# Performance work log

Measured on AMD Instinct MI355X. Metric: run time of the kernel, lower is better.

## Reference

```python
import jax, jax.numpy as jnp
import numpy as np

NUM_NODES = 100000
EMBED_DIM = 128
HIDDEN = 128
NUM_EDGES = 1600000


def gcn_conv(x, W, b, src, dst, num_nodes):
    """PyG GCNConv: x' = D^{-1/2} (A+I) D^{-1/2} (x W) + b, symmetric norm with self-loops."""
    x = x @ W  # [N, out]
    loops = jnp.arange(num_nodes, dtype=src.dtype)
    s = jnp.concatenate([src, loops])  # sources incl. self-loops
    d = jnp.concatenate([dst, loops])  # targets incl. self-loops
    deg = jax.ops.segment_sum(jnp.ones_like(d, dtype=x.dtype), d, num_segments=num_nodes)
    dis = jnp.where(deg > 0, jax.lax.rsqrt(deg), 0.0)  # deg^{-1/2}, 0 where isolated
    norm = dis[s] * dis[d]  # [E+N]
    msg = x[s] * norm[:, None]  # gather + scale
    out = jax.ops.segment_sum(msg, d, num_segments=num_nodes)  # scatter-add
    return out + b


def setup_inputs() -> dict:
    key = jax.random.key(0)
    k1, k2, k3, k4, k5, k6 = jax.random.split(key, 6)
    edge_index = jax.random.randint(k1, (2, NUM_EDGES), 0, NUM_NODES, dtype=jnp.int64)
    edge_attr = jax.random.normal(k2, (NUM_EDGES,), dtype=jnp.float32)
    emb = jax.random.normal(k3, (NUM_NODES, EMBED_DIM), dtype=jnp.float32) * 0.1
    W1 = jax.random.normal(k4, (EMBED_DIM, HIDDEN), dtype=jnp.float32) * (1.0 / np.sqrt(EMBED_DIM))
    b1 = jnp.zeros((HIDDEN,), dtype=jnp.float32)
    W2 = jax.random.normal(k5, (HIDDEN, HIDDEN), dtype=jnp.float32) * (1.0 / np.sqrt(HIDDEN))
    b2 = jnp.zeros((HIDDEN,), dtype=jnp.float32)
    return {"edge_index": edge_index, "edge_attr": edge_attr, "emb": emb,
            "W1": W1, "b1": b1, "W2": W2, "b2": b2}


def reference(edge_index, edge_attr, emb, W1, b1, W2, b2):
    src, dst = edge_index[0], edge_index[1]
    x = gcn_conv(emb, W1, b1, src, dst, NUM_NODES)
    x = jax.nn.relu(x)
    x = gcn_conv(x, W2, b2, src, dst, NUM_NODES)
    return x
```

## Files before the change

kernel.cpp:

```cpp
#include <hip/hip_runtime.h>

#define EMB 128
#define NBUC 1024
#define NPART 256
#define PREPB 128

typedef __attribute__((ext_vector_type(8))) short short8;
typedef __attribute__((ext_vector_type(4))) float f32x4;

__device__ __forceinline__ unsigned short f2bf(float f) {
    union { float f; unsigned int i; } v; v.f = f;
    unsigned int x = v.i;
    x += 0x7fffu + ((x >> 16) & 1u);
    return (unsigned short)(x >> 16);
}
__device__ __forceinline__ void acc_fma4(uint2 v, float d,
                                         float& a0, float& a1, float& a2, float& a3) {
    union { unsigned int i; float f; } t;
    t.i = v.x << 16;          a0 = fmaf(d, t.f, a0);
    t.i = v.x & 0xffff0000u;  a1 = fmaf(d, t.f, a1);
    t.i = v.y << 16;          a2 = fmaf(d, t.f, a2);
    t.i = v.y & 0xffff0000u;  a3 = fmaf(d, t.f, a3);
}
__device__ __forceinline__ void acc_bf4(uint2 v,
                                        float& a0, float& a1, float& a2, float& a3) {
    union { unsigned int i; float f; } t;
    t.i = v.x << 16;          a0 += t.f;
    t.i = v.x & 0xffff0000u;  a1 += t.f;
    t.i = v.y << 16;          a2 += t.f;
    t.i = v.y & 0xffff0000u;  a3 += t.f;
}


__device__ __forceinline__ void p1_body(int bid, int* h, const int* __restrict__ dst,
                                        int* __restrict__ tot, int E, int chunk) {
    for (int i = threadIdx.x; i < NBUC; i += 256) h[i] = 0;
    __syncthreads();
    int s = bid * chunk;
    int e = min(E, s + chunk);
    for (int i = s + threadIdx.x; i < e; i += 256)
        atomicAdd(&h[dst[i] >> 7], 1);
    __syncthreads();
    for (int i = threadIdx.x; i < NBUC; i += 256) {
        int v = h[i];
        if (v) atomicAdd(&tot[i], v);
    }
}

__device__ __forceinline__ void prepw_body(int bid, const float* __restrict__ W1,
                                           const float* __restrict__ W2,
                                           unsigned short* __restrict__ W1s,
                                           unsigned short* __restrict__ W2s) {
    int gid = bid * 256 + threadIdx.x;
    const float* W = (gid < 16384) ? W1 : W2;
    unsigned short* Ws = (gid < 16384) ? W1s : W2s;
    int idx = gid & 16383;
    int k = idx >> 7, n = idx & 127;
    int kk = k >> 5, q = (k >> 3) & 3, j = k & 7;
    int ct = n >> 4, nn = n & 15;
    int didx = ((((kk * 8 + ct) * 4 + q) * 16 + nn) << 3) + j;
    Ws[didx] = f2bf(W[idx]);
}

__global__ __launch_bounds__(256) void k_start(const int* __restrict__ dst,
                                               int* __restrict__ tot, int E, int chunk,
                                               const float* __restrict__ W1,
                                               const float* __restrict__ W2,
                                               unsigned short* __restrict__ W1s,
                                               unsigned short* __restrict__ W2s) {
    __shared__ int h[NBUC];
    int b = blockIdx.x;
    if (b < NPART) p1_body(b, h, dst, tot, E, chunk);
    else           prepw_body(b - NPART, W1, W2, W1s, W2s);
}

__global__ __launch_bounds__(1024) void p_scan(const int* __restrict__ tot,
                                               int* __restrict__ base,
                                               int* __restrict__ gcnt, int E) {
    __shared__ int a[NBUC];
    int t = threadIdx.x;
    int v0 = tot[t];
    a[t] = v0;
    __syncthreads();
    for (int off = 1; off < NBUC; off <<= 1) {
        int v = (t >= off) ? a[t - off] : 0;
        __syncthreads();
        a[t] += v;
        __syncthreads();
    }
    int excl = a[t] - v0;
    base[t] = excl;
    gcnt[t] = excl;
    if (t == NBUC - 1) base[NBUC] = E;
}

__device__ __forceinline__ void scatter_body(int bid, int* cnt,
                                             const int* __restrict__ src,
                                             const int* __restrict__ dst,
                                             int* __restrict__ gcnt,
                                             int* __restrict__ part,
                                             int E, int chunk) {
    for (int i = threadIdx.x; i < NBUC; i += 256) cnt[i] = 0;
    __syncthreads();
    int s = bid * chunk;
    int e = min(E, s + chunk);
    for (int i = s + threadIdx.x; i < e; i += 256)
        atomicAdd(&cnt[dst[i] >> 7], 1);
    __syncthreads();
    for (int i = threadIdx.x; i < NBUC; i += 256) {
        int c = cnt[i];
        cnt[i] = c ? atomicAdd(&gcnt[i], c) : 0;
    }
    __syncthreads();
    for (int i = s + threadIdx.x; i < e; i += 256) {
        int d = dst[i];
        int pos = atomicAdd(&cnt[d >> 7], 1);
        part[pos] = src[i] | ((d & 127) << 17);
    }
}

__global__ __launch_bounds__(256) void p3_csr(const int* __restrict__ part,
                                              const int* __restrict__ base,
                                              int* __restrict__ R, int* __restrict__ adj,
                                              float* __restrict__ dis, int N, int E) {
    __shared__ int hist[128];
    __shared__ int sc[128];
    __shared__ int cnt[128];
    int b = blockIdx.x;
    int n0 = b * 128;
    int nn = min(128, N - n0);
    int s = base[b], e = base[b + 1];
    int t = threadIdx.x;

    if (t < 128) hist[t] = 0;
    __syncthreads();
    for (int i = s + t; i < e; i += 256)
        atomicAdd(&hist[part[i] >> 17], 1);
    __syncthreads();

    if (t < 128) sc[t] = hist[t];
    __syncthreads();
    for (int off = 1; off < 128; off <<= 1) {
        int v = 0;
        if (t < 128 && t >= off) v = sc[t - off];
        __syncthreads();
        if (t < 128) sc[t] += v;
        __syncthreads();
    }
    if (t < 128) {
        int excl = sc[t] - hist[t];
        cnt[t] = excl;
        if (t < nn) {
            R[n0 + t] = s + excl;
            dis[n0 + t] = rsqrtf((float)hist[t] + 1.0f);
        }
    }
    if (b == 0 && t == 0) R[N] = E;
    __syncthreads();

    for (int i = s + t; i < e; i += 256) {
        int p = part[i];
        int pos = atomicAdd(&cnt[p >> 17], 1);
        adj[s + pos] = p & 0x1FFFF;
    }
}

template <bool XBF16, bool SCALE>
__device__ __forceinline__ void gemm_body(int bid, unsigned short* lds,
    const void* Xv, const unsigned short* __restrict__ Wsw,
    const float* __restrict__ dis, unsigned short* __restrict__ Y, int N)
{
    {
        const uint4* srcp = (const uint4*)Wsw;
        uint4* dstp = (uint4*)lds;
        for (int i = threadIdx.x; i < 2048; i += 256) dstp[i] = srcp[i];
    }
    __syncthreads();

    const int wave = threadIdx.x >> 6;
    const int lane = threadIdx.x & 63;
    const int q = lane >> 4, nn = lane & 15;
    const int row0 = bid * 64 + wave * 16;
    const int arow = row0 + nn;
    const int arc = arow < N ? arow : N - 1;

    f32x4 acc[8];
#pragma unroll
    for (int ct = 0; ct < 8; ++ct) acc[ct] = (f32x4){0.f, 0.f, 0.f, 0.f};

#pragma unroll
    for (int kk = 0; kk < 4; ++kk) {
        short8 af;
        if (XBF16) {
            af = *(const short8*)((const unsigned short*)Xv + (size_t)arc * EMB + kk * 32 + q * 8);
        } else {
            const float* xp = (const float*)Xv + (size_t)arc * EMB + kk * 32 + q * 8;
            float4 u0 = *(const float4*)xp;
            float4 u1 = *(const float4*)(xp + 4);
            af[0] = (short)f2bf(u0.x); af[1] = (short)f2bf(u0.y);
            af[2] = (short)f2bf(u0.z); af[3] = (short)f2bf(u0.w);
            af[4] = (short)f2bf(u1.x); af[5] = (short)f2bf(u1.y);
            af[6] = (short)f2bf(u1.z); af[7] = (short)f2bf(u1.w);
        }
#pragma unroll
        for (int ct = 0; ct < 8; ++ct) {
            short8 bf = ((const short8*)lds)[(kk * 8 + ct) * 64 + lane];
            acc[ct] = __builtin_amdgcn_mfma_f32_16x16x32_bf16(af, bf, acc[ct], 0, 0, 0);
        }
    }

    __syncthreads();

    float dv[4];
    if (SCALE) {
#pragma unroll
        for (int r = 0; r < 4; ++r) {
            int gm = row0 + q * 4 + r;
            dv[r] = dis[gm < N ? gm : N - 1];
        }
    }
#pragma unroll
    for (int ct = 0; ct < 8; ++ct) {
#pragma unroll
        for (int r = 0; r < 4; ++r) {
            int ml = wave * 16 + q * 4 + r;
            float val = SCALE ? acc[ct][r] * dv[r] : acc[ct][r];
            lds[ml * 136 + ct * 16 + nn] = f2bf(val);
        }
    }
    __syncthreads();

    const int rbase = bid * 64;
    for (int i = threadIdx.x; i < 1024; i += 256) {
        int row = i >> 4, off = i & 15;
        int grow = rbase + row;
        if (grow < N) {
            uint4 v = *(const uint4*)(lds + row * 136 + off * 8);
            *((uint4*)(Y + (size_t)grow * EMB) + off) = v;
        }
    }
}

__global__ __launch_bounds__(256) void k_mid(
    const int* __restrict__ src, const int* __restrict__ dstp,
    int* __restrict__ gcnt, int* __restrict__ part, int E, int chunk,
    const void* Xv, const unsigned short* __restrict__ W1s,
    unsigned short* __restrict__ Y, int N)
{
    __shared__ __align__(16) unsigned short smem[16384];
    int b = blockIdx.x;
    if (b < NPART) scatter_body(b, (int*)smem, src, dstp, gcnt, part, E, chunk);
    else           gemm_body<false, false>(b - NPART, smem, Xv, W1s, nullptr, Y, N);
}

__global__ __launch_bounds__(256) void k_gemm2(
    const void* Xv, const unsigned short* __restrict__ Wsw,
    const float* __restrict__ dis, unsigned short* __restrict__ Y, int N)
{
    __shared__ __align__(16) unsigned short smem[16384];
    gemm_body<true, true>(blockIdx.x, smem, Xv, Wsw, dis, Y, N);
}

template <bool FOLD, bool RELU, bool BF16OUT>
__global__ __launch_bounds__(256) void k_gather_split(
    const int* __restrict__ R, const int* __restrict__ adj,
    const unsigned short* __restrict__ Y, const float* __restrict__ dis,
    const float* __restrict__ bias, void* __restrict__ Outv, int N, int half)
{
    int bid = blockIdx.x;
    int pass = (bid >= half) ? 1 : 0;
    int t = (bid - pass * half) * 256 + threadIdx.x;
    int n = t >> 4;
    if (n >= N) return;
    int j = pass * 64 + (t & 15) * 4;

    int rs = R[n], re = R[n + 1];
    float dv = dis[n];

    float a0 = 0.f, a1 = 0.f, a2 = 0.f, a3 = 0.f;
    uint2 sv = *(const uint2*)(Y + (size_t)n * EMB + j);
    if (FOLD) acc_fma4(sv, dv, a0, a1, a2, a3);
    else      acc_bf4(sv, a0, a1, a2, a3);

    int e = rs;
    for (; e + 3 < re; e += 4) {
        int s0 = adj[e], s1 = adj[e + 1], s2 = adj[e + 2], s3 = adj[e + 3];
        uint2 v0 = *(const uint2*)(Y + (size_t)s0 * EMB + j);
        uint2 v1 = *(const uint2*)(Y + (size_t)s1 * EMB + j);
        uint2 v2 = *(const uint2*)(Y + (size_t)s2 * EMB + j);
        uint2 v3 = *(const uint2*)(Y + (size_t)s3 * EMB + j);
        if (FOLD) {
            float d0 = dis[s0], d1 = dis[s1], d2 = dis[s2], d3 = dis[s3];
            acc_fma4(v0, d0, a0, a1, a2, a3); acc_fma4(v1, d1, a0, a1, a2, a3);
            acc_fma4(v2, d2, a0, a1, a2, a3); acc_fma4(v3, d3, a0, a1, a2, a3);
        } else {
            acc_bf4(v0, a0, a1, a2, a3); acc_bf4(v1, a0, a1, a2, a3);
            acc_bf4(v2, a0, a1, a2, a3); acc_bf4(v3, a0, a1, a2, a3);
        }
    }
    for (; e < re; ++e) {
        int s0 = adj[e];
        uint2 v0 = *(const uint2*)(Y + (size_t)s0 * EMB + j);
        if (FOLD) acc_fma4(v0, dis[s0], a0, a1, a2, a3);
        else      acc_bf4(v0, a0, a1, a2, a3);
    }

    float4 b = *(const float4*)(bias + j);
    float o0 = dv * a0 + b.x;
    float o1 = dv * a1 + b.y;
    float o2 = dv * a2 + b.z;
    float o3 = dv * a3 + b.w;
    if (RELU) {
        o0 = fmaxf(o0, 0.f); o1 = fmaxf(o1, 0.f);
        o2 = fmaxf(o2, 0.f); o3 = fmaxf(o3, 0.f);
    }
    if (BF16OUT) {
        ushort4 o = { f2bf(o0), f2bf(o1), f2bf(o2), f2bf(o3) };
        *(ushort4*)((unsigned short*)Outv + (size_t)n * EMB + j) = o;
    } else {
        float4 o = { o0, o1, o2, o3 };
        *(float4*)((float*)Outv + (size_t)n * EMB + j) = o;
    }
}

extern "C" void kernel_launch(void* const* d_in, const int* in_sizes, int n_in,
                              void* d_out, int out_size, void* d_ws, size_t ws_size,
                              hipStream_t stream) {
    const int* ei = (const int*)d_in[0];
    const int E = in_sizes[0] / 2;
    const float* emb = (const float*)d_in[2];
    const int N = in_sizes[2] / EMB;
    const float* W1 = (const float*)d_in[3];
    const float* b1 = (const float*)d_in[4];
    const float* W2 = (const float*)d_in[5];
    const float* b2 = (const float*)d_in[6];
    float* out = (float*)d_out;

    const int* src = ei;
    const int* dstp = ei + E;

    char* w = (char*)d_ws;
    auto take = [&](size_t bytes) { char* p = w; w += (bytes + 511) & ~(size_t)511; return p; };
    float* dis  = (float*)take((size_t)N * 4);
    int*   R    = (int*)  take((size_t)(N + 1) * 4);
    int*   base = (int*)  take((size_t)(NBUC + 1) * 4);
    int*   tot  = (int*)  take((size_t)NBUC * 4);
    int*   gcnt = (int*)  take((size_t)NBUC * 4);
    int*   adj  = (int*)  take((size_t)E * 4);
    unsigned short* W1s = (unsigned short*)take((size_t)EMB * EMB * 2);
    unsigned short* W2s = (unsigned short*)take((size_t)EMB * EMB * 2);
    unsigned short* Hb  = (unsigned short*)take((size_t)N * EMB * 2);
    int*   part = (int*)Hb;
    unsigned short* Y1b = (unsigned short*)d_out;

    const int NB = (N + 127) / 128;
    const int chunk = (E + NPART - 1) / NPART;
    const int gM = (N + 63) / 64;
    const int half = (N * 16 + 255) / 256;
    const int gG = 2 * half;

    hipMemsetAsync(tot, 0, (size_t)NBUC * 4, stream);

    k_start<<<NPART + PREPB, 256, 0, stream>>>(dstp, tot, E, chunk, W1, W2, W1s, W2s);

    p_scan<<<1, NBUC, 0, stream>>>(tot, base, gcnt, E);

    k_mid<<<NPART + gM, 256, 0, stream>>>(src, dstp, gcnt, part, E, chunk,
                                          emb, W1s, Y1b, N);

    p3_csr<<<NB, 256, 0, stream>>>(part, base, R, adj, dis, N, E);

    k_gather_split<true, true, true><<<gG, 256, 0, stream>>>(R, adj, Y1b, dis, b1, Hb, N, half);

    k_gemm2<<<gM, 256, 0, stream>>>(Hb, W2s, dis, Hb, N);
    k_gather_split<false, false, false><<<gG, 256, 0, stream>>>(R, adj, Hb, dis, b2, out, N, half);
}
```

Before: 325.6 us.

## Fuse first-layer aggregation with second GEMM and widen gathers to full rows

The layer-1 gather, bias and ReLU now feed straight into the layer-2 MFMA GEMM inside one kernel, with the 16-node hidden tile kept in LDS. This removes the separate GEMM launch and the round trip of the hidden activations through global memory. Both gathers also drop the two-pass half-row split: each thread now loads 16-byte uint4 chunks covering a full 128-wide row, so each adjacency list is read once instead of twice. In exchange there are fewer threads per node column, only 16 rows per block for the MFMA, and W2 fragments are held in registers, which may raise register pressure.

```diff
diff --git a/kernel.cpp b/kernel.cpp
--- a/kernel.cpp
+++ b/kernel.cpp
@@ -14,21 +14,27 @@
     x += 0x7fffu + ((x >> 16) & 1u);
     return (unsigned short)(x >> 16);
 }
-__device__ __forceinline__ void acc_fma4(uint2 v, float d,
-                                         float& a0, float& a1, float& a2, float& a3) {
+__device__ __forceinline__ void acc_fma8(uint4 v, float d, float* a) {
     union { unsigned int i; float f; } t;
-    t.i = v.x << 16;          a0 = fmaf(d, t.f, a0);
-    t.i = v.x & 0xffff0000u;  a1 = fmaf(d, t.f, a1);
-    t.i = v.y << 16;          a2 = fmaf(d, t.f, a2);
-    t.i = v.y & 0xffff0000u;  a3 = fmaf(d, t.f, a3);
-}
-__device__ __forceinline__ void acc_bf4(uint2 v,
-                                        float& a0, float& a1, float& a2, float& a3) {
+    t.i = v.x << 16;          a[0] = fmaf(d, t.f, a[0]);
+    t.i = v.x & 0xffff0000u;  a[1] = fmaf(d, t.f, a[1]);
+    t.i = v.y << 16;          a[2] = fmaf(d, t.f, a[2]);
+    t.i = v.y & 0xffff0000u;  a[3] = fmaf(d, t.f, a[3]);
+    t.i = v.z << 16;          a[4] = fmaf(d, t.f, a[4]);
+    t.i = v.z & 0xffff0000u;  a[5] = fmaf(d, t.f, a[5]);
+    t.i = v.w << 16;          a[6] = fmaf(d, t.f, a[6]);
+    t.i = v.w & 0xffff0000u;  a[7] = fmaf(d, t.f, a[7]);
+}
+__device__ __forceinline__ void acc_add8(uint4 v, float* a) {
     union { unsigned int i; float f; } t;
-    t.i = v.x << 16;          a0 += t.f;
-    t.i = v.x & 0xffff0000u;  a1 += t.f;
-    t.i = v.y << 16;          a2 += t.f;
-    t.i = v.y & 0xffff0000u;  a3 += t.f;
+    t.i = v.x << 16;          a[0] += t.f;
+    t.i = v.x & 0xffff0000u;  a[1] += t.f;
+    t.i = v.y << 16;          a[2] += t.f;
+    t.i = v.y & 0xffff0000u;  a[3] += t.f;
+    t.i = v.z << 16;          a[4] += t.f;
+    t.i = v.z & 0xffff0000u;  a[5] += t.f;
+    t.i = v.w << 16;          a[6] += t.f;
+    t.i = v.w & 0xffff0000u;  a[7] += t.f;
 }
 
 
@@ -165,10 +171,9 @@
     }
 }
 
-template <bool XBF16, bool SCALE>
 __device__ __forceinline__ void gemm_body(int bid, unsigned short* lds,
-    const void* Xv, const unsigned short* __restrict__ Wsw,
-    const float* __restrict__ dis, unsigned short* __restrict__ Y, int N)
+    const float* __restrict__ Xv, const unsigned short* __restrict__ Wsw,
+    unsigned short* __restrict__ Y, int N)
 {
     {
         const uint4* srcp = (const uint4*)Wsw;
@@ -190,18 +195,14 @@
 
 #pragma unroll
     for (int kk = 0; kk < 4; ++kk) {
+        const float* xp = Xv + (size_t)arc * EMB + kk * 32 + q * 8;
+        float4 u0 = *(const float4*)xp;
+        float4 u1 = *(const float4*)(xp + 4);
         short8 af;
-        if (XBF16) {
-            af = *(const short8*)((const unsigned short*)Xv + (size_t)arc * EMB + kk * 32 + q * 8);
-        } else {
-            const float* xp = (const float*)Xv + (size_t)arc * EMB + kk * 32 + q * 8;
-            float4 u0 = *(const float4*)xp;
-            float4 u1 = *(const float4*)(xp + 4);
-            af[0] = (short)f2bf(u0.x); af[1] = (short)f2bf(u0.y);
-            af[2] = (short)f2bf(u0.z); af[3] = (short)f2bf(u0.w);
-            af[4] = (short)f2bf(u1.x); af[5] = (short)f2bf(u1.y);
-            af[6] = (short)f2bf(u1.z); af[7] = (short)f2bf(u1.w);
-        }
+        af[0] = (short)f2bf(u0.x); af[1] = (short)f2bf(u0.y);
+        af[2] = (short)f2bf(u0.z); af[3] = (short)f2bf(u0.w);
+        af[4] = (short)f2bf(u1.x); af[5] = (short)f2bf(u1.y);
+        af[6] = (short)f2bf(u1.z); af[7] = (short)f2bf(u1.w);
 #pragma unroll
         for (int ct = 0; ct < 8; ++ct) {
             short8 bf = ((const short8*)lds)[(kk * 8 + ct) * 64 + lane];
@@ -211,21 +212,12 @@
 
     __syncthreads();
 
-    float dv[4];
-    if (SCALE) {
-#pragma unroll
-        for (int r = 0; r < 4; ++r) {
-            int gm = row0 + q * 4 + r;
-            dv[r] = dis[gm < N ? gm : N - 1];
-        }
-    }
 #pragma unroll
     for (int ct = 0; ct < 8; ++ct) {
 #pragma unroll
         for (int r = 0; r < 4; ++r) {
             int ml = wave * 16 + q * 4 + r;
-            float val = SCALE ? acc[ct][r] * dv[r] : acc[ct][r];
-            lds[ml * 136 + ct * 16 + nn] = f2bf(val);
+            lds[ml * 136 + ct * 16 + nn] = f2bf(acc[ct][r]);
         }
     }
     __syncthreads();
@@ -244,83 +236,164 @@
 __global__ __launch_bounds__(256) void k_mid(
     const int* __restrict__ src, const int* __restrict__ dstp,
     int* __restrict__ gcnt, int* __restrict__ part, int E, int chunk,
-    const void* Xv, const unsigned short* __restrict__ W1s,
+    const float* __restrict__ Xv, const unsigned short* __restrict__ W1s,
     unsigned short* __restrict__ Y, int N)
 {
     __shared__ __align__(16) unsigned short smem[16384];
     int b = blockIdx.x;
     if (b < NPART) scatter_body(b, (int*)smem, src, dstp, gcnt, part, E, chunk);
-    else           gemm_body<false, false>(b - NPART, smem, Xv, W1s, nullptr, Y, N);
-}
-
-__global__ __launch_bounds__(256) void k_gemm2(
-    const void* Xv, const unsigned short* __restrict__ Wsw,
-    const float* __restrict__ dis, unsigned short* __restrict__ Y, int N)
+    else           gemm_body(b - NPART, smem, Xv, W1s, Y, N);
+}
+
+__global__ __launch_bounds__(256) void k_gather_gemm(
+    const int* __restrict__ R, const int* __restrict__ adj,
+    const unsigned short* __restrict__ Y1, const float* __restrict__ dis,
+    const float* __restrict__ b1, const unsigned short* __restrict__ W2s,
+    unsigned short* __restrict__ Y2, int N)
 {
-    __shared__ __align__(16) unsigned short smem[16384];
-    gemm_body<true, true>(blockIdx.x, smem, Xv, Wsw, dis, Y, N);
-}
-
-template <bool FOLD, bool RELU, bool BF16OUT>
-__global__ __launch_bounds__(256) void k_gather_split(
+    __shared__ __align__(16) unsigned short Hs[16][136];
+
+    const int wave = threadIdx.x >> 6;
+    const int lane = threadIdx.x & 63;
+    const int q = lane >> 4, nn = lane & 15;
+
+    short8 bfrag[8];
+#pragma unroll
+    for (int kk = 0; kk < 4; ++kk)
+#pragma unroll
+        for (int c = 0; c < 2; ++c) {
+            int ct = wave * 2 + c;
+            bfrag[kk * 2 + c] =
+                *(const short8*)(W2s + ((((kk * 8 + ct) * 4 + q) * 16 + nn) << 3));
+        }
+
+    const int nl = threadIdx.x >> 4;
+    const int n  = blockIdx.x * 16 + nl;
+    const int j  = (threadIdx.x & 15) * 8;
+    const bool valid = n < N;
+
+    float a[8];
+#pragma unroll
+    for (int k = 0; k < 8; ++k) a[k] = 0.f;
+
+    if (valid) {
+        float dv = dis[n];
+        uint4 sv = *(const uint4*)(Y1 + (size_t)n * EMB + j);
+        acc_fma8(sv, dv, a);
+
+        int e = R[n];
+        const int re = R[n + 1];
+        for (; e + 3 < re; e += 4) {
+            int s0 = adj[e], s1 = adj[e + 1], s2 = adj[e + 2], s3 = adj[e + 3];
+            float d0 = dis[s0], d1 = dis[s1], d2 = dis[s2], d3 = dis[s3];
+            uint4 v0 = *(const uint4*)(Y1 + (size_t)s0 * EMB + j);
+            uint4 v1 = *(const uint4*)(Y1 + (size_t)s1 * EMB + j);
+            uint4 v2 = *(const uint4*)(Y1 + (size_t)s2 * EMB + j);
+            uint4 v3 = *(const uint4*)(Y1 + (size_t)s3 * EMB + j);
+            acc_fma8(v0, d0, a); acc_fma8(v1, d1, a);
+            acc_fma8(v2, d2, a); acc_fma8(v3, d3, a);
+        }
+        for (; e < re; ++e) {
+            int s0 = adj[e];
+            uint4 v0 = *(const uint4*)(Y1 + (size_t)s0 * EMB + j);
+            acc_fma8(v0, dis[s0], a);
+        }
+
+        float4 bb0 = *(const float4*)(b1 + j);
+        float4 bb1 = *(const float4*)(b1 + j + 4);
+        a[0] = fmaxf(dv * a[0] + bb0.x, 0.f);
+        a[1] = fmaxf(dv * a[1] + bb0.y, 0.f);
+        a[2] = fmaxf(dv * a[2] + bb0.z, 0.f);
+        a[3] = fmaxf(dv * a[3] + bb0.w, 0.f);
+        a[4] = fmaxf(dv * a[4] + bb1.x, 0.f);
+        a[5] = fmaxf(dv * a[5] + bb1.y, 0.f);
+        a[6] = fmaxf(dv * a[6] + bb1.z, 0.f);
+        a[7] = fmaxf(dv * a[7] + bb1.w, 0.f);
+    }
+
+    {
+        uint4 pk;
+        pk.x = (unsigned)f2bf(a[0]) | ((unsigned)f2bf(a[1]) << 16);
+        pk.y = (unsigned)f2bf(a[2]) | ((unsigned)f2bf(a[3]) << 16);
+        pk.z = (unsigned)f2bf(a[4]) | ((unsigned)f2bf(a[5]) << 16);
+        pk.w = (unsigned)f2bf(a[6]) | ((unsigned)f2bf(a[7]) << 16);
+        *(uint4*)(&Hs[nl][j]) = pk;
+    }
+    __syncthreads();
+
+    f32x4 acc0 = (f32x4){0.f, 0.f, 0.f, 0.f};
+    f32x4 acc1 = (f32x4){0.f, 0.f, 0.f, 0.f};
+#pragma unroll
+    for (int kk = 0; kk < 4; ++kk) {
+        short8 af = *(const short8*)(&Hs[nn][kk * 32 + q * 8]);
+        acc0 = __builtin_amdgcn_mfma_f32_16x16x32_bf16(af, bfrag[kk * 2 + 0], acc0, 0, 0, 0);
+        acc1 = __builtin_amdgcn_mfma_f32_16x16x32_bf16(af, bfrag[kk * 2 + 1], acc1, 0, 0, 0);
+    }
+    __syncthreads();
+
+    const int ct0 = wave * 2, ct1 = wave * 2 + 1;
+#pragma unroll
+    for (int r = 0; r < 4; ++r) {
+        int m = q * 4 + r;
+        int gm = blockIdx.x * 16 + m;
+        float dm = dis[gm < N ? gm : N - 1];
+        Hs[m][ct0 * 16 + nn] = f2bf(acc0[r] * dm);
+        Hs[m][ct1 * 16 + nn] = f2bf(acc1[r] * dm);
+    }
+    __syncthreads();
+
+    {
+        int row = threadIdx.x >> 4, off = threadIdx.x & 15;
+        int gr = blockIdx.x * 16 + row;
+        if (gr < N) {
+            uint4 v = *(const uint4*)(&Hs[row][off * 8]);
+            *((uint4*)(Y2 + (size_t)gr * EMB) + off) = v;
+        }
+    }
+}
+
+__global__ __launch_bounds__(256) void k_gather_out(
     const int* __restrict__ R, const int* __restrict__ adj,
     const unsigned short* __restrict__ Y, const float* __restrict__ dis,
-    const float* __restrict__ bias, void* __restrict__ Outv, int N, int half)
+    const float* __restrict__ bias, float* __restrict__ out, int N)
 {
-    int bid = blockIdx.x;
-    int pass = (bid >= half) ? 1 : 0;
-    int t = (bid - pass * half) * 256 + threadIdx.x;
+    int t = blockIdx.x * 256 + threadIdx.x;
     int n = t >> 4;
     if (n >= N) return;
-    int j = pass * 64 + (t & 15) * 4;
-
-    int rs = R[n], re = R[n + 1];
-    float dv = dis[n];
-
-    float a0 = 0.f, a1 = 0.f, a2 = 0.f, a3 = 0.f;
-    uint2 sv = *(const uint2*)(Y + (size_t)n * EMB + j);
-    if (FOLD) acc_fma4(sv, dv, a0, a1, a2, a3);
-    else      acc_bf4(sv, a0, a1, a2, a3);
-
-    int e = rs;
+    int j = (t & 15) * 8;
+
+    float a[8];
+#pragma unroll
+    for (int k = 0; k < 8; ++k) a[k] = 0.f;
+
+    uint4 sv = *(const uint4*)(Y + (size_t)n * EMB + j);
+    acc_add8(sv, a);
+
+    int e = R[n];
+    const int re = R[n + 1];
     for (; e + 3 < re; e += 4) {
         int s0 = adj[e], s1 = adj[e + 1], s2 = adj[e + 2], s3 = adj[e + 3];
-        uint2 v0 = *(const uint2*)(Y + (size_t)s0 * EMB + j);
-        uint2 v1 = *(const uint2*)(Y + (size_t)s1 * EMB + j);
-        uint2 v2 = *(const uint2*)(Y + (size_t)s2 * EMB + j);
-        uint2 v3 = *(const uint2*)(Y + (size_t)s3 * EMB + j);
-        if (FOLD) {
-            float d0 = dis[s0], d1 = dis[s1], d2 = dis[s2], d3 = dis[s3];
-            acc_fma4(v0, d0, a0, a1, a2, a3); acc_fma4(v1, d1, a0, a1, a2, a3);
-            acc_fma4(v2, d2, a0, a1, a2, a3); acc_fma4(v3, d3, a0, a1, a2, a3);
-        } else {
-            acc_bf4(v0, a0, a1, a2, a3); acc_bf4(v1, a0, a1, a2, a3);
-            acc_bf4(v2, a0, a1, a2, a3); acc_bf4(v3, a0, a1, a2, a3);
-        }
+        uint4 v0 = *(const uint4*)(Y + (size_t)s0 * EMB + j);
+        uint4 v1 = *(const uint4*)(Y + (size_t)s1 * EMB + j);
+        uint4 v2 = *(const uint4*)(Y + (size_t)s2 * EMB + j);
+        uint4 v3 = *(const uint4*)(Y + (size_t)s3 * EMB + j);
+        acc_add8(v0, a); acc_add8(v1, a); acc_add8(v2, a); acc_add8(v3, a);
     }
     for (; e < re; ++e) {
-        int s0 = adj[e];
-        uint2 v0 = *(const uint2*)(Y + (size_t)s0 * EMB + j);
-        if (FOLD) acc_fma4(v0, dis[s0], a0, a1, a2, a3);
-        else      acc_bf4(v0, a0, a1, a2, a3);
-    }
-
-    float4 b = *(const float4*)(bias + j);
-    float o0 = dv * a0 + b.x;
-    float o1 = dv * a1 + b.y;
-    float o2 = dv * a2 + b.z;
-    float o3 = dv * a3 + b.w;
-    if (RELU) {
-        o0 = fmaxf(o0, 0.f); o1 = fmaxf(o1, 0.f);
-        o2 = fmaxf(o2, 0.f); o3 = fmaxf(o3, 0.f);
-    }
-    if (BF16OUT) {
-        ushort4 o = { f2bf(o0), f2bf(o1), f2bf(o2), f2bf(o3) };
-        *(ushort4*)((unsigned short*)Outv + (size_t)n * EMB + j) = o;
-    } else {
-        float4 o = { o0, o1, o2, o3 };
-        *(float4*)((float*)Outv + (size_t)n * EMB + j) = o;
-    }
+        uint4 v0 = *(const uint4*)(Y + (size_t)adj[e] * EMB + j);
+        acc_add8(v0, a);
+    }
+
+    const float dv = dis[n];
+    float4 bb0 = *(const float4*)(bias + j);
+    float4 bb1 = *(const float4*)(bias + j + 4);
+    float4 o0 = { dv * a[0] + bb0.x, dv * a[1] + bb0.y,
+                  dv * a[2] + bb0.z, dv * a[3] + bb0.w };
+    float4 o1 = { dv * a[4] + bb1.x, dv * a[5] + bb1.y,
+                  dv * a[6] + bb1.z, dv * a[7] + bb1.w };
+    float* op = out + (size_t)n * EMB + j;
+    *(float4*)op = o0;
+    *(float4*)(op + 4) = o1;
 }
 
 extern "C" void kernel_launch(void* const* d_in, const int* in_sizes, int n_in,
@@ -349,15 +422,15 @@
     int*   adj  = (int*)  take((size_t)E * 4);
     unsigned short* W1s = (unsigned short*)take((size_t)EMB * EMB * 2);
     unsigned short* W2s = (unsigned short*)take((size_t)EMB * EMB * 2);
-    unsigned short* Hb  = (unsigned short*)take((size_t)N * EMB * 2);
-    int*   part = (int*)Hb;
+    unsigned short* Y2b = (unsigned short*)take((size_t)N * EMB * 2);
+    int*   part = (int*)Y2b;
     unsigned short* Y1b = (unsigned short*)d_out;
 
     const int NB = (N + 127) / 128;
     const int chunk = (E + NPART - 1) / NPART;
     const int gM = (N + 63) / 64;
-    const int half = (N * 16 + 255) / 256;
-    const int gG = 2 * half;
+    const int gF = (N + 15) / 16;
+    const int gG = (N * 16 + 255) / 256;
 
     hipMemsetAsync(tot, 0, (size_t)NBUC * 4, stream);
 
@@ -370,8 +443,7 @@
 
     p3_csr<<<NB, 256, 0, stream>>>(part, base, R, adj, dis, N, E);
 
-    k_gather_split<true, true, true><<<gG, 256, 0, stream>>>(R, adj, Y1b, dis, b1, Hb, N, half);
-
-    k_gemm2<<<gM, 256, 0, stream>>>(Hb, W2s, dis, Hb, N);
-    k_gather_split<false, false, false><<<gG, 256, 0, stream>>>(R, adj, Hb, dis, b2, out, N, half);
-}
+    k_gather_gemm<<<gF, 256, 0, stream>>>(R, adj, Y1b, dis, b1, W2s, Y2b, N);
+
+    k_gather_out<<<gG, 256, 0, stream>>>(R, adj, Y2b, dis, b2, out, N);
+}
```

Measured after the change: 320.3 us. No clear change (-1.6%).

## Fuse whole GCN pipeline into one persistent cooperative kernel with grid syncs

Applied to the files above, without the earlier changes.

Replaces the seven separate launches plus memset with one cooperative persistent kernel that steps through the phases (histogram, scan, scatter plus GEMM1, CSR build, gather1 fused with GEMM2, gather2) separated by grid-wide syncs. Gather1 is fused with the second GEMM per 16-row tile through LDS, so the intermediate H no longer makes a round trip through global memory. It also reads W fragments straight from global memory instead of staging them in LDS. The aim is to remove launch gaps and a full intermediate pass. The costs are grid-sync overhead, lower occupancy from 512-thread blocks, and small per-tile MFMA work in the fused phase.

```diff
diff --git a/kernel.cpp b/kernel.cpp
--- a/kernel.cpp
+++ b/kernel.cpp
@@ -1,9 +1,11 @@
 #include <hip/hip_runtime.h>
+#include <hip/hip_cooperative_groups.h>
+
+namespace cg = cooperative_groups;
 
 #define EMB 128
 #define NBUC 1024
-#define NPART 256
-#define PREPB 128
+#define PWB 64
 
 typedef __attribute__((ext_vector_type(8))) short short8;
 typedef __attribute__((ext_vector_type(4))) float f32x4;
@@ -31,295 +33,300 @@
     t.i = v.y & 0xffff0000u;  a3 += t.f;
 }
 
-
-__device__ __forceinline__ void p1_body(int bid, int* h, const int* __restrict__ dst,
-                                        int* __restrict__ tot, int E, int chunk) {
-    for (int i = threadIdx.x; i < NBUC; i += 256) h[i] = 0;
-    __syncthreads();
-    int s = bid * chunk;
-    int e = min(E, s + chunk);
-    for (int i = s + threadIdx.x; i < e; i += 256)
-        atomicAdd(&h[dst[i] >> 7], 1);
-    __syncthreads();
-    for (int i = threadIdx.x; i < NBUC; i += 256) {
-        int v = h[i];
-        if (v) atomicAdd(&tot[i], v);
-    }
-}
-
-__device__ __forceinline__ void prepw_body(int bid, const float* __restrict__ W1,
-                                           const float* __restrict__ W2,
-                                           unsigned short* __restrict__ W1s,
-                                           unsigned short* __restrict__ W2s) {
-    int gid = bid * 256 + threadIdx.x;
-    const float* W = (gid < 16384) ? W1 : W2;
-    unsigned short* Ws = (gid < 16384) ? W1s : W2s;
-    int idx = gid & 16383;
-    int k = idx >> 7, n = idx & 127;
-    int kk = k >> 5, q = (k >> 3) & 3, j = k & 7;
-    int ct = n >> 4, nn = n & 15;
-    int didx = ((((kk * 8 + ct) * 4 + q) * 16 + nn) << 3) + j;
-    Ws[didx] = f2bf(W[idx]);
-}
-
-__global__ __launch_bounds__(256) void k_start(const int* __restrict__ dst,
-                                               int* __restrict__ tot, int E, int chunk,
-                                               const float* __restrict__ W1,
-                                               const float* __restrict__ W2,
-                                               unsigned short* __restrict__ W1s,
-                                               unsigned short* __restrict__ W2s) {
-    __shared__ int h[NBUC];
-    int b = blockIdx.x;
-    if (b < NPART) p1_body(b, h, dst, tot, E, chunk);
-    else           prepw_body(b - NPART, W1, W2, W1s, W2s);
-}
-
-__global__ __launch_bounds__(1024) void p_scan(const int* __restrict__ tot,
-                                               int* __restrict__ base,
-                                               int* __restrict__ gcnt, int E) {
-    __shared__ int a[NBUC];
-    int t = threadIdx.x;
-    int v0 = tot[t];
-    a[t] = v0;
-    __syncthreads();
-    for (int off = 1; off < NBUC; off <<= 1) {
-        int v = (t >= off) ? a[t - off] : 0;
-        __syncthreads();
-        a[t] += v;
-        __syncthreads();
-    }
-    int excl = a[t] - v0;
-    base[t] = excl;
-    gcnt[t] = excl;
-    if (t == NBUC - 1) base[NBUC] = E;
-}
-
-__device__ __forceinline__ void scatter_body(int bid, int* cnt,
-                                             const int* __restrict__ src,
-                                             const int* __restrict__ dst,
-                                             int* __restrict__ gcnt,
-                                             int* __restrict__ part,
-                                             int E, int chunk) {
-    for (int i = threadIdx.x; i < NBUC; i += 256) cnt[i] = 0;
-    __syncthreads();
-    int s = bid * chunk;
-    int e = min(E, s + chunk);
-    for (int i = s + threadIdx.x; i < e; i += 256)
-        atomicAdd(&cnt[dst[i] >> 7], 1);
-    __syncthreads();
-    for (int i = threadIdx.x; i < NBUC; i += 256) {
-        int c = cnt[i];
-        cnt[i] = c ? atomicAdd(&gcnt[i], c) : 0;
-    }
-    __syncthreads();
-    for (int i = s + threadIdx.x; i < e; i += 256) {
-        int d = dst[i];
-        int pos = atomicAdd(&cnt[d >> 7], 1);
-        part[pos] = src[i] | ((d & 127) << 17);
-    }
-}
-
-__global__ __launch_bounds__(256) void p3_csr(const int* __restrict__ part,
-                                              const int* __restrict__ base,
-                                              int* __restrict__ R, int* __restrict__ adj,
-                                              float* __restrict__ dis, int N, int E) {
-    __shared__ int hist[128];
-    __shared__ int sc[128];
-    __shared__ int cnt[128];
-    int b = blockIdx.x;
-    int n0 = b * 128;
-    int nn = min(128, N - n0);
-    int s = base[b], e = base[b + 1];
-    int t = threadIdx.x;
-
-    if (t < 128) hist[t] = 0;
-    __syncthreads();
-    for (int i = s + t; i < e; i += 256)
-        atomicAdd(&hist[part[i] >> 17], 1);
-    __syncthreads();
-
-    if (t < 128) sc[t] = hist[t];
-    __syncthreads();
-    for (int off = 1; off < 128; off <<= 1) {
-        int v = 0;
-        if (t < 128 && t >= off) v = sc[t - off];
-        __syncthreads();
-        if (t < 128) sc[t] += v;
-        __syncthreads();
-    }
-    if (t < 128) {
-        int excl = sc[t] - hist[t];
-        cnt[t] = excl;
-        if (t < nn) {
-            R[n0 + t] = s + excl;
-            dis[n0 + t] = rsqrtf((float)hist[t] + 1.0f);
-        }
-    }
-    if (b == 0 && t == 0) R[N] = E;
-    __syncthreads();
-
-    for (int i = s + t; i < e; i += 256) {
-        int p = part[i];
-        int pos = atomicAdd(&cnt[p >> 17], 1);
-        adj[s + pos] = p & 0x1FFFF;
-    }
-}
-
-template <bool XBF16, bool SCALE>
-__device__ __forceinline__ void gemm_body(int bid, unsigned short* lds,
-    const void* Xv, const unsigned short* __restrict__ Wsw,
-    const float* __restrict__ dis, unsigned short* __restrict__ Y, int N)
+__global__ __launch_bounds__(512, 8) void k_all(
+    const int* __restrict__ src, const int* __restrict__ dst, int E,
+    const float* __restrict__ emb,
+    const float* __restrict__ W1, const float* __restrict__ b1,
+    const float* __restrict__ W2, const float* __restrict__ b2,
+    float* __restrict__ out, int N,
+    int* __restrict__ tot, int* __restrict__ base, int* __restrict__ gcnt,
+    int* __restrict__ R, int* __restrict__ adj, float* __restrict__ dis,
+    unsigned short* __restrict__ W1s, unsigned short* __restrict__ W2s,
+    int* __restrict__ part,
+    unsigned short* __restrict__ Y1, unsigned short* __restrict__ Y2)
 {
+    cg::grid_group g = cg::this_grid();
+    __shared__ __align__(16) char smem[17408];
+    const int tid = threadIdx.x;
+    const int bid = blockIdx.x;
+    const int nb  = gridDim.x;
+    const int wave = tid >> 6;
+    const int lane = tid & 63;
+    const int q = lane >> 4, nn = lane & 15;
+
     {
-        const uint4* srcp = (const uint4*)Wsw;
-        uint4* dstp = (uint4*)lds;
-        for (int i = threadIdx.x; i < 2048; i += 256) dstp[i] = srcp[i];
-    }
-    __syncthreads();
-
-    const int wave = threadIdx.x >> 6;
-    const int lane = threadIdx.x & 63;
-    const int q = lane >> 4, nn = lane & 15;
-    const int row0 = bid * 64 + wave * 16;
-    const int arow = row0 + nn;
-    const int arc = arow < N ? arow : N - 1;
-
-    f32x4 acc[8];
-#pragma unroll
-    for (int ct = 0; ct < 8; ++ct) acc[ct] = (f32x4){0.f, 0.f, 0.f, 0.f};
-
-#pragma unroll
-    for (int kk = 0; kk < 4; ++kk) {
-        short8 af;
-        if (XBF16) {
-            af = *(const short8*)((const unsigned short*)Xv + (size_t)arc * EMB + kk * 32 + q * 8);
-        } else {
-            const float* xp = (const float*)Xv + (size_t)arc * EMB + kk * 32 + q * 8;
-            float4 u0 = *(const float4*)xp;
-            float4 u1 = *(const float4*)(xp + 4);
-            af[0] = (short)f2bf(u0.x); af[1] = (short)f2bf(u0.y);
-            af[2] = (short)f2bf(u0.z); af[3] = (short)f2bf(u0.w);
-            af[4] = (short)f2bf(u1.x); af[5] = (short)f2bf(u1.y);
-            af[6] = (short)f2bf(u1.z); af[7] = (short)f2bf(u1.w);
-        }
-#pragma unroll
-        for (int ct = 0; ct < 8; ++ct) {
-            short8 bf = ((const short8*)lds)[(kk * 8 + ct) * 64 + lane];
-            acc[ct] = __builtin_amdgcn_mfma_f32_16x16x32_bf16(af, bf, acc[ct], 0, 0, 0);
-        }
-    }
-
-    __syncthreads();
-
-    float dv[4];
-    if (SCALE) {
-#pragma unroll
-        for (int r = 0; r < 4; ++r) {
-            int gm = row0 + q * 4 + r;
-            dv[r] = dis[gm < N ? gm : N - 1];
-        }
-    }
-#pragma unroll
-    for (int ct = 0; ct < 8; ++ct) {
-#pragma unroll
-        for (int r = 0; r < 4; ++r) {
-            int ml = wave * 16 + q * 4 + r;
-            float val = SCALE ? acc[ct][r] * dv[r] : acc[ct][r];
-            lds[ml * 136 + ct * 16 + nn] = f2bf(val);
-        }
-    }
-    __syncthreads();
-
-    const int rbase = bid * 64;
-    for (int i = threadIdx.x; i < 1024; i += 256) {
-        int row = i >> 4, off = i & 15;
-        int grow = rbase + row;
-        if (grow < N) {
-            uint4 v = *(const uint4*)(lds + row * 136 + off * 8);
-            *((uint4*)(Y + (size_t)grow * EMB) + off) = v;
-        }
-    }
-}
-
-__global__ __launch_bounds__(256) void k_mid(
-    const int* __restrict__ src, const int* __restrict__ dstp,
-    int* __restrict__ gcnt, int* __restrict__ part, int E, int chunk,
-    const void* Xv, const unsigned short* __restrict__ W1s,
-    unsigned short* __restrict__ Y, int N)
-{
-    __shared__ __align__(16) unsigned short smem[16384];
-    int b = blockIdx.x;
-    if (b < NPART) scatter_body(b, (int*)smem, src, dstp, gcnt, part, E, chunk);
-    else           gemm_body<false, false>(b - NPART, smem, Xv, W1s, nullptr, Y, N);
-}
-
-__global__ __launch_bounds__(256) void k_gemm2(
-    const void* Xv, const unsigned short* __restrict__ Wsw,
-    const float* __restrict__ dis, unsigned short* __restrict__ Y, int N)
-{
-    __shared__ __align__(16) unsigned short smem[16384];
-    gemm_body<true, true>(blockIdx.x, smem, Xv, Wsw, dis, Y, N);
-}
-
-template <bool FOLD, bool RELU, bool BF16OUT>
-__global__ __launch_bounds__(256) void k_gather_split(
-    const int* __restrict__ R, const int* __restrict__ adj,
-    const unsigned short* __restrict__ Y, const float* __restrict__ dis,
-    const float* __restrict__ bias, void* __restrict__ Outv, int N, int half)
-{
-    int bid = blockIdx.x;
-    int pass = (bid >= half) ? 1 : 0;
-    int t = (bid - pass * half) * 256 + threadIdx.x;
-    int n = t >> 4;
-    if (n >= N) return;
-    int j = pass * 64 + (t & 15) * 4;
-
-    int rs = R[n], re = R[n + 1];
-    float dv = dis[n];
-
-    float a0 = 0.f, a1 = 0.f, a2 = 0.f, a3 = 0.f;
-    uint2 sv = *(const uint2*)(Y + (size_t)n * EMB + j);
-    if (FOLD) acc_fma4(sv, dv, a0, a1, a2, a3);
-    else      acc_bf4(sv, a0, a1, a2, a3);
-
-    int e = rs;
-    for (; e + 3 < re; e += 4) {
-        int s0 = adj[e], s1 = adj[e + 1], s2 = adj[e + 2], s3 = adj[e + 3];
-        uint2 v0 = *(const uint2*)(Y + (size_t)s0 * EMB + j);
-        uint2 v1 = *(const uint2*)(Y + (size_t)s1 * EMB + j);
-        uint2 v2 = *(const uint2*)(Y + (size_t)s2 * EMB + j);
-        uint2 v3 = *(const uint2*)(Y + (size_t)s3 * EMB + j);
-        if (FOLD) {
-            float d0 = dis[s0], d1 = dis[s1], d2 = dis[s2], d3 = dis[s3];
-            acc_fma4(v0, d0, a0, a1, a2, a3); acc_fma4(v1, d1, a0, a1, a2, a3);
-            acc_fma4(v2, d2, a0, a1, a2, a3); acc_fma4(v3, d3, a0, a1, a2, a3);
-        } else {
-            acc_bf4(v0, a0, a1, a2, a3); acc_bf4(v1, a0, a1, a2, a3);
-            acc_bf4(v2, a0, a1, a2, a3); acc_bf4(v3, a0, a1, a2, a3);
-        }
-    }
-    for (; e < re; ++e) {
-        int s0 = adj[e];
-        uint2 v0 = *(const uint2*)(Y + (size_t)s0 * EMB + j);
-        if (FOLD) acc_fma4(v0, dis[s0], a0, a1, a2, a3);
-        else      acc_bf4(v0, a0, a1, a2, a3);
-    }
-
-    float4 b = *(const float4*)(bias + j);
-    float o0 = dv * a0 + b.x;
-    float o1 = dv * a1 + b.y;
-    float o2 = dv * a2 + b.z;
-    float o3 = dv * a3 + b.w;
-    if (RELU) {
-        o0 = fmaxf(o0, 0.f); o1 = fmaxf(o1, 0.f);
-        o2 = fmaxf(o2, 0.f); o3 = fmaxf(o3, 0.f);
-    }
-    if (BF16OUT) {
-        ushort4 o = { f2bf(o0), f2bf(o1), f2bf(o2), f2bf(o3) };
-        *(ushort4*)((unsigned short*)Outv + (size_t)n * EMB + j) = o;
+        int i = bid * 512 + tid;
+        if (i < NBUC) tot[i] = 0;
+    }
+    g.sync();
+
+    if (bid < PWB) {
+        int gid = bid * 512 + tid;
+        const float* W = (gid < 16384) ? W1 : W2;
+        unsigned short* Ws = (gid < 16384) ? W1s : W2s;
+        int idx = gid & 16383;
+        int k = idx >> 7, n = idx & 127;
+        int kk = k >> 5, qq = (k >> 3) & 3, j = k & 7;
+        int ct = n >> 4, n2 = n & 15;
+        Ws[((((kk * 8 + ct) * 4 + qq) * 16 + n2) << 3) + j] = f2bf(W[idx]);
     } else {
-        float4 o = { o0, o1, o2, o3 };
-        *(float4*)((float*)Outv + (size_t)n * EMB + j) = o;
+        int* h = (int*)smem;
+        for (int i = tid; i < NBUC; i += 512) h[i] = 0;
+        __syncthreads();
+        int nhb = nb - PWB;
+        int chunk = (E + nhb - 1) / nhb;
+        int s = (bid - PWB) * chunk, e = min(E, s + chunk);
+        for (int i = s + tid; i < e; i += 512)
+            atomicAdd(&h[dst[i] >> 7], 1);
+        __syncthreads();
+        for (int i = tid; i < NBUC; i += 512) {
+            int v = h[i];
+            if (v) atomicAdd(&tot[i], v);
+        }
+    }
+    g.sync();
+
+    if (bid == 0) {
+        int* a = (int*)smem;
+        int v0 = tot[2 * tid], v1 = tot[2 * tid + 1];
+        int sp = v0 + v1;
+        a[tid] = sp;
+        __syncthreads();
+        for (int off = 1; off < 512; off <<= 1) {
+            int v = (tid >= off) ? a[tid - off] : 0;
+            __syncthreads();
+            a[tid] += v;
+            __syncthreads();
+        }
+        int ex = a[tid] - sp;
+        base[2 * tid] = ex;         gcnt[2 * tid] = ex;
+        base[2 * tid + 1] = ex + v0; gcnt[2 * tid + 1] = ex + v0;
+        if (tid == 511) base[NBUC] = E;
+    }
+    g.sync();
+
+    const int SCB = nb >> 1;
+    if (bid < SCB) {
+        int* cnt = (int*)smem;
+        for (int i = tid; i < NBUC; i += 512) cnt[i] = 0;
+        __syncthreads();
+        int chunk = (E + SCB - 1) / SCB;
+        int s = bid * chunk, e = min(E, s + chunk);
+        for (int i = s + tid; i < e; i += 512)
+            atomicAdd(&cnt[dst[i] >> 7], 1);
+        __syncthreads();
+        for (int i = tid; i < NBUC; i += 512) {
+            int c = cnt[i];
+            cnt[i] = c ? atomicAdd(&gcnt[i], c) : 0;
+        }
+        __syncthreads();
+        for (int i = s + tid; i < e; i += 512) {
+            int d = dst[i];
+            int pos = atomicAdd(&cnt[d >> 7], 1);
+            part[pos] = src[i] | ((d & 127) << 17);
+        }
+    } else {
+        int ntile = (N + 127) >> 7;
+        unsigned short* lds = (unsigned short*)smem;
+        for (int tile = bid - SCB; tile < ntile; tile += nb - SCB) {
+            int row0 = (tile << 7) + wave * 16;
+            int arow = row0 + nn;
+            int arc = arow < N ? arow : N - 1;
+            f32x4 acc[8];
+#pragma unroll
+            for (int ct = 0; ct < 8; ++ct) acc[ct] = (f32x4){0.f, 0.f, 0.f, 0.f};
+#pragma unroll
+            for (int kk = 0; kk < 4; ++kk) {
+                const float* xp = emb + (size_t)arc * EMB + kk * 32 + q * 8;
+                float4 u0 = *(const float4*)xp;
+                float4 u1 = *(const float4*)(xp + 4);
+                short8 af;
+                af[0] = (short)f2bf(u0.x); af[1] = (short)f2bf(u0.y);
+                af[2] = (short)f2bf(u0.z); af[3] = (short)f2bf(u0.w);
+                af[4] = (short)f2bf(u1.x); af[5] = (short)f2bf(u1.y);
+                af[6] = (short)f2bf(u1.z); af[7] = (short)f2bf(u1.w);
+#pragma unroll
+                for (int ct = 0; ct < 8; ++ct) {
+                    short8 bf = *(const short8*)(W1s +
+                        ((((kk * 8 + ct) * 4 + q) * 16 + nn) << 3));
+                    acc[ct] = __builtin_amdgcn_mfma_f32_16x16x32_bf16(af, bf, acc[ct], 0, 0, 0);
+                }
+            }
+#pragma unroll
+            for (int half = 0; half < 2; ++half) {
+                __syncthreads();
+                if ((wave >> 2) == half) {
+                    int wl = wave & 3;
+#pragma unroll
+                    for (int ct = 0; ct < 8; ++ct)
+#pragma unroll
+                        for (int r = 0; r < 4; ++r)
+                            lds[(wl * 16 + q * 4 + r) * 136 + ct * 16 + nn] =
+                                f2bf(acc[ct][r]);
+                }
+                __syncthreads();
+                int rbase = (tile << 7) + half * 64;
+                for (int i = tid; i < 1024; i += 512) {
+                    int row = i >> 4, off = i & 15;
+                    int grow = rbase + row;
+                    if (grow < N)
+                        *((uint4*)(Y1 + (size_t)grow * EMB) + off) =
+                            *(const uint4*)(lds + row * 136 + off * 8);
+                }
+            }
+            __syncthreads();
+        }
+    }
+    g.sync();
+
+    {
+        int nbuck = (N + 127) >> 7;
+        int* hist = (int*)smem;
+        int* sc   = hist + 128;
+        int* cnt  = sc + 128;
+        for (int b = bid; b < nbuck; b += nb) {
+            int n0 = b << 7;
+            int nn2 = min(128, N - n0);
+            int s = base[b], e = base[b + 1];
+            if (tid < 128) hist[tid] = 0;
+            __syncthreads();
+            for (int i = s + tid; i < e; i += 512)
+                atomicAdd(&hist[part[i] >> 17], 1);
+            __syncthreads();
+            if (tid < 128) sc[tid] = hist[tid];
+            __syncthreads();
+            for (int off = 1; off < 128; off <<= 1) {
+                int v = 0;
+                if (tid < 128 && tid >= off) v = sc[tid - off];
+                __syncthreads();
+                if (tid < 128) sc[tid] += v;
+                __syncthreads();
+            }
+            if (tid < 128) {
+                int ex = sc[tid] - hist[tid];
+                cnt[tid] = ex;
+                if (tid < nn2) {
+                    R[n0 + tid] = s + ex;
+                    dis[n0 + tid] = rsqrtf((float)hist[tid] + 1.0f);
+                }
+            }
+            if (b == 0 && tid == 0) R[N] = E;
+            __syncthreads();
+            for (int i = s + tid; i < e; i += 512) {
+                int p = part[i];
+                int pos = atomicAdd(&cnt[p >> 17], 1);
+                adj[s + pos] = p & 0x1FFFF;
+            }
+            __syncthreads();
+        }
+    }
+    g.sync();
+
+    {
+        int ntile = (N + 15) >> 4;
+        unsigned short* Hs = (unsigned short*)smem;
+        const int nl = tid >> 5;
+        const int lj = (tid & 31) * 4;
+        for (int tile = bid; tile < ntile; tile += nb) {
+            int n = (tile << 4) + nl;
+            float a0 = 0.f, a1 = 0.f, a2 = 0.f, a3 = 0.f;
+            if (n < N) {
+                float dv = dis[n];
+                uint2 sv = *(const uint2*)(Y1 + (size_t)n * EMB + lj);
+                acc_fma4(sv, dv, a0, a1, a2, a3);
+                int e = R[n];
+                const int re = R[n + 1];
+                for (; e + 3 < re; e += 4) {
+                    int s0 = adj[e], s1 = adj[e + 1], s2 = adj[e + 2], s3 = adj[e + 3];
+                    float d0 = dis[s0], d1 = dis[s1], d2 = dis[s2], d3 = dis[s3];
+                    uint2 v0 = *(const uint2*)(Y1 + (size_t)s0 * EMB + lj);
+                    uint2 v1 = *(const uint2*)(Y1 + (size_t)s1 * EMB + lj);
+                    uint2 v2 = *(const uint2*)(Y1 + (size_t)s2 * EMB + lj);
+                    uint2 v3 = *(const uint2*)(Y1 + (size_t)s3 * EMB + lj);
+                    acc_fma4(v0, d0, a0, a1, a2, a3);
+                    acc_fma4(v1, d1, a0, a1, a2, a3);
+                    acc_fma4(v2, d2, a0, a1, a2, a3);
+                    acc_fma4(v3, d3, a0, a1, a2, a3);
+                }
+                for (; e < re; ++e) {
+                    int s0 = adj[e];
+                    uint2 v0 = *(const uint2*)(Y1 + (size_t)s0 * EMB + lj);
+                    acc_fma4(v0, dis[s0], a0, a1, a2, a3);
+                }
+                float4 bb = *(const float4*)(b1 + lj);
+                a0 = fmaxf(dv * a0 + bb.x, 0.f);
+                a1 = fmaxf(dv * a1 + bb.y, 0.f);
+                a2 = fmaxf(dv * a2 + bb.z, 0.f);
+                a3 = fmaxf(dv * a3 + bb.w, 0.f);
+            }
+            uint2 pk;
+            pk.x = (unsigned)f2bf(a0) | ((unsigned)f2bf(a1) << 16);
+            pk.y = (unsigned)f2bf(a2) | ((unsigned)f2bf(a3) << 16);
+            *(uint2*)(Hs + nl * 136 + lj) = pk;
+            __syncthreads();
+
+            f32x4 acc = (f32x4){0.f, 0.f, 0.f, 0.f};
+#pragma unroll
+            for (int kk = 0; kk < 4; ++kk) {
+                short8 af = *(const short8*)(Hs + nn * 136 + kk * 32 + q * 8);
+                short8 bf = *(const short8*)(W2s +
+                    ((((kk * 8 + wave) * 4 + q) * 16 + nn) << 3));
+                acc = __builtin_amdgcn_mfma_f32_16x16x32_bf16(af, bf, acc, 0, 0, 0);
+            }
+            __syncthreads();
+
+#pragma unroll
+            for (int r = 0; r < 4; ++r) {
+                int m = q * 4 + r;
+                int gm = (tile << 4) + m;
+                float dm = dis[gm < N ? gm : N - 1];
+                Hs[m * 136 + wave * 16 + nn] = f2bf(acc[r] * dm);
+            }
+            __syncthreads();
+
+            {
+                int row = tid >> 5, off = tid & 31;
+                int gr = (tile << 4) + row;
+                if (gr < N)
+                    *((uint2*)(Y2 + (size_t)gr * EMB) + off) =
+                        *(const uint2*)(Hs + row * 136 + off * 4);
+            }
+            __syncthreads();
+        }
+    }
+    g.sync();
+
+    {
+        int nch = (N + 15) >> 4;
+        const int nl = tid >> 5;
+        const int lj = (tid & 31) * 4;
+        for (int ch = bid; ch < nch; ch += nb) {
+            int n = (ch << 4) + nl;
+            if (n >= N) continue;
+            float a0 = 0.f, a1 = 0.f, a2 = 0.f, a3 = 0.f;
+            uint2 sv = *(const uint2*)(Y2 + (size_t)n * EMB + lj);
+            acc_bf4(sv, a0, a1, a2, a3);
+            int e = R[n];
+            const int re = R[n + 1];
+            for (; e + 3 < re; e += 4) {
+                int s0 = adj[e], s1 = adj[e + 1], s2 = adj[e + 2], s3 = adj[e + 3];
+                uint2 v0 = *(const uint2*)(Y2 + (size_t)s0 * EMB + lj);
+                uint2 v1 = *(const uint2*)(Y2 + (size_t)s1 * EMB + lj);
+                uint2 v2 = *(const uint2*)(Y2 + (size_t)s2 * EMB + lj);
+                uint2 v3 = *(const uint2*)(Y2 + (size_t)s3 * EMB + lj);
+                acc_bf4(v0, a0, a1, a2, a3); acc_bf4(v1, a0, a1, a2, a3);
+                acc_bf4(v2, a0, a1, a2, a3); acc_bf4(v3, a0, a1, a2, a3);
+            }
+            for (; e < re; ++e) {
+                uint2 v0 = *(const uint2*)(Y2 + (size_t)adj[e] * EMB + lj);
+                acc_bf4(v0, a0, a1, a2, a3);
+            }
+            float dv = dis[n];
+            float4 bb = *(const float4*)(b2 + lj);
+            float4 o = { dv * a0 + bb.x, dv * a1 + bb.y,
+                         dv * a2 + bb.z, dv * a3 + bb.w };
+            *(float4*)(out + (size_t)n * EMB + lj) = o;
+        }
     }
 }
 
@@ -327,9 +334,9 @@
                               void* d_out, int out_size, void* d_ws, size_t ws_size,
                               hipStream_t stream) {
     const int* ei = (const int*)d_in[0];
-    const int E = in_sizes[0] / 2;
+    int E = in_sizes[0] / 2;
     const float* emb = (const float*)d_in[2];
-    const int N = in_sizes[2] / EMB;
+    int N = in_sizes[2] / EMB;
     const float* W1 = (const float*)d_in[3];
     const float* b1 = (const float*)d_in[4];
     const float* W2 = (const float*)d_in[5];
@@ -349,29 +356,27 @@
     int*   adj  = (int*)  take((size_t)E * 4);
     unsigned short* W1s = (unsigned short*)take((size_t)EMB * EMB * 2);
     unsigned short* W2s = (unsigned short*)take((size_t)EMB * EMB * 2);
-    unsigned short* Hb  = (unsigned short*)take((size_t)N * EMB * 2);
-    int*   part = (int*)Hb;
-    unsigned short* Y1b = (unsigned short*)d_out;
-
-    const int NB = (N + 127) / 128;
-    const int chunk = (E + NPART - 1) / NPART;
-    const int gM = (N + 63) / 64;
-    const int half = (N * 16 + 255) / 256;
-    const int gG = 2 * half;
-
-    hipMemsetAsync(tot, 0, (size_t)NBUC * 4, stream);
-
-    k_start<<<NPART + PREPB, 256, 0, stream>>>(dstp, tot, E, chunk, W1, W2, W1s, W2s);
-
-    p_scan<<<1, NBUC, 0, stream>>>(tot, base, gcnt, E);
-
-    k_mid<<<NPART + gM, 256, 0, stream>>>(src, dstp, gcnt, part, E, chunk,
-                                          emb, W1s, Y1b, N);
-
-    p3_csr<<<NB, 256, 0, stream>>>(part, base, R, adj, dis, N, E);
-
-    k_gather_split<true, true, true><<<gG, 256, 0, stream>>>(R, adj, Y1b, dis, b1, Hb, N, half);
-
-    k_gemm2<<<gM, 256, 0, stream>>>(Hb, W2s, dis, Hb, N);
-    k_gather_split<false, false, false><<<gG, 256, 0, stream>>>(R, adj, Hb, dis, b2, out, N, half);
-}
+    unsigned short* Y2  = (unsigned short*)take((size_t)N * EMB * 2);
+    int*   part = (int*)Y2;
+    unsigned short* Y1 = (unsigned short*)d_out;
+
+    static int maxb = -1;
+    if (maxb < 0) {
+        hipOccupancyMaxActiveBlocksPerMultiprocessor(&maxb, (const void*)k_all, 512, 0);
+        if (maxb < 1) maxb = 1;
+    }
+    int nb = maxb * 256;
+    if (nb > 1024) nb = 1024;
+    if (nb < 128) nb = 128;
+
+    void* args[] = {
+        (void*)&src, (void*)&dstp, (void*)&E, (void*)&emb,
+        (void*)&W1, (void*)&b1, (void*)&W2, (void*)&b2,
+        (void*)&out, (void*)&N,
+        (void*)&tot, (void*)&base, (void*)&gcnt,
+        (void*)&R, (void*)&adj, (void*)&dis,
+        (void*)&W1s, (void*)&W2s, (void*)&part,
+        (void*)&Y1, (void*)&Y2
+    };
+    hipLaunchCooperativeKernel((void*)k_all, dim3(nb), dim3(512), args, 0, stream);
+}
```

Result: slower. 755.5 us (+132.0%).
